# Performance work log

Measured on AMD Instinct MI355X. Metric: run time of the kernel, lower is better.

Reference implementation:

```python
import jax, jax.numpy as jnp
import numpy as np

CAPACITY_FACTOR = 1.0

def setup_inputs() -> dict:
    key = jax.random.key(0)
    ks = jax.random.split(key, 5)
    B, S, D, E, F = 2, 2048, 1024, 8, 4096
    x = jax.random.normal(ks[0], (B, S, D), dtype=jnp.float32)
    Ws = jax.random.normal(ks[1], (D, E), dtype=jnp.float32) * (1.0 / np.sqrt(D))
    bs = jnp.zeros((E,), dtype=jnp.float32)
    W1 = jax.random.normal(ks[2], (E, D, F), dtype=jnp.float32) * (1.0 / np.sqrt(D))
    b1 = jnp.zeros((E, F), dtype=jnp.float32)
    W2 = jax.random.normal(ks[3], (E, F, D), dtype=jnp.float32) * (1.0 / np.sqrt(F))
    b2 = jnp.zeros((E, D), dtype=jnp.float32)
    return {"x": x, "Ws": Ws, "bs": bs, "W1": W1, "b1": b1, "W2": W2, "b2": b2}

def reference(x, Ws, bs, W1, b1, W2, b2):
    B, S, D = x.shape
    E = Ws.shape[1]
    N = B * S
    k = int(CAPACITY_FACTOR * N / E)  # expert-choice capacity
    xf = x.reshape(N, D)
    # switch gating: [N, E] -> [E, N]
    route_prob = jax.nn.softmax(xf @ Ws + bs, axis=-1).T
    # expert-choice top-k tokens per expert: values/indices [E, k]
    route_vals, routes = jax.lax.top_k(route_prob, k)
    # dispatch: gather per-expert token blocks [E, k, D]
    xin = xf[routes]
    # per-expert FFN (grouped GEMM): Linear -> GELU -> Linear
    h = jax.nn.gelu(jnp.einsum('ekd,edf->ekf', xin, W1) + b1[:, None, :])
    out = jnp.einsum('ekf,efd->ekd', h, W2) + b2[:, None, :]
    # scale by routing prob (is_scale_prob=True)
    out = out * route_vals[..., None]
    # combine: scatter-add into token buffer (== sum over the E-indexed zero tensor)
    final = jnp.zeros((N, D), dtype=x.dtype).at[routes.reshape(-1)].add(out.reshape(-1, D))
    return final.reshape(B, S, D)
```

## Files before the change

### kernel.cpp

```cpp
#include <hip/hip_runtime.h>
#include <hip/hip_bf16.h>

#define N_TOK 4096
#define DIM   1024
#define NEXP  8
#define FDIM  4096
#define KCAP  512

typedef __attribute__((ext_vector_type(8))) short bf16x8;
typedef __attribute__((ext_vector_type(4))) float floatx4;

__device__ inline unsigned short f2bf(float f) {
  union { float f; unsigned int i; } v; v.f = f;
  unsigned int r = v.i + 0x7fffu + ((v.i >> 16) & 1u);
  return (unsigned short)(r >> 16);
}

__device__ inline void ld2lds16(const void* g, void* l) {
  __builtin_amdgcn_global_load_lds(
      (const __attribute__((address_space(1))) unsigned int*)g,
      (__attribute__((address_space(3))) unsigned int*)l,
      16, 0, 0);
}

__device__ inline void transpose64(const float* __restrict__ src,
                                   unsigned short* __restrict__ dst,
                                   int R, int C, int e, int by, int bx, int t,
                                   unsigned short (*tile)[66]) {
  size_t off = (size_t)e * R * C;
  int r0 = by * 64, c0 = bx * 64;
  const float* S = src + off + (size_t)r0 * C + c0;
#pragma unroll
  for (int p = 0; p < 4; p++) {
    int r = (t >> 4) + p * 16, c = (t & 15) * 4;
    float4 v = *(const float4*)&S[(size_t)r * C + c];
    tile[r][c + 0] = f2bf(v.x);
    tile[r][c + 1] = f2bf(v.y);
    tile[r][c + 2] = f2bf(v.z);
    tile[r][c + 3] = f2bf(v.w);
  }
  __syncthreads();
  unsigned short* D = dst + off + (size_t)c0 * R + r0;
#pragma unroll
  for (int p = 0; p < 2; p++) {
    int oc = (t >> 3) + p * 32;
    int orr = (t & 7) * 8;
    bf16x8 o;
#pragma unroll
    for (int j = 0; j < 8; j++) o[j] = (short)tile[orr + j][oc];
    *(bf16x8*)&D[(size_t)oc * R + orr] = o;
  }
}

__global__ __launch_bounds__(256)
void prep_kernel(const float* __restrict__ x,
                 const float* __restrict__ Ws,
                 const float* __restrict__ bs,
                 float* __restrict__ probs_t,
                 unsigned short* __restrict__ xb,
                 const float* __restrict__ W1, unsigned short* __restrict__ wt) {
  __shared__ unsigned short tile[64][66];
  int bid = blockIdx.x;
  int t = threadIdx.x;

  if (bid >= 1024) {
    int b = bid - 1024;
    int e = b >> 10, rem = b & 1023;
    int bx = rem & 63, by = rem >> 6;
    transpose64(W1, wt, DIM, FDIM, e, by, bx, t, tile);
    return;
  }

  int token = bid * 4 + (t >> 6);
  int lane  = t & 63;
  const float* xr = x + (size_t)token * DIM;
  unsigned short* xbr = xb + (size_t)token * DIM;
  double acc[NEXP];
#pragma unroll
  for (int e = 0; e < NEXP; e++) acc[e] = 0.0;
#pragma unroll
  for (int c = 0; c < 4; c++) {
    int d0 = (c * 64 + lane) * 4;
    float4 xv = *(const float4*)&xr[d0];
    ushort4 ob;
    ob.x = f2bf(xv.x); ob.y = f2bf(xv.y); ob.z = f2bf(xv.z); ob.w = f2bf(xv.w);
    *(ushort4*)&xbr[d0] = ob;
    float xa[4] = {xv.x, xv.y, xv.z, xv.w};
#pragma unroll
    for (int q = 0; q < 4; q++) {
      const float* wr = &Ws[(size_t)(d0 + q) * NEXP];
      float4 w0 = *(const float4*)&wr[0];
      float4 w1 = *(const float4*)&wr[4];
      double xs = (double)xa[q];
      acc[0] += xs * (double)w0.x; acc[1] += xs * (double)w0.y;
      acc[2] += xs * (double)w0.z; acc[3] += xs * (double)w0.w;
      acc[4] += xs * (double)w1.x; acc[5] += xs * (double)w1.y;
      acc[6] += xs * (double)w1.z; acc[7] += xs * (double)w1.w;
    }
  }
#pragma unroll
  for (int off = 32; off > 0; off >>= 1)
#pragma unroll
    for (int e = 0; e < NEXP; e++) acc[e] += __shfl_down(acc[e], off, 64);
  if (lane == 0) {
    double mx = -1e300;
#pragma unroll
    for (int e = 0; e < NEXP; e++) { acc[e] += (double)bs[e]; if (acc[e] > mx) mx = acc[e]; }
    double s = 0.0, p[NEXP];
#pragma unroll
    for (int e = 0; e < NEXP; e++) { p[e] = exp(acc[e] - mx); s += p[e]; }
#pragma unroll
    for (int e = 0; e < NEXP; e++) probs_t[(size_t)e * N_TOK + token] = (float)(p[e] / s);
  }
}

__global__ __launch_bounds__(256)
void t2_kernel(const float* __restrict__ W2, unsigned short* __restrict__ wt) {
  __shared__ unsigned short tile[64][66];
  int b = blockIdx.x, t = threadIdx.x;
  int e = b >> 10, rem = b & 1023;
  int bx = rem & 15, by = rem >> 4;
  transpose64(W2, wt, FDIM, DIM, e, by, bx, t, tile);
}

__global__ __launch_bounds__(1024)
void topk_kernel(const float* __restrict__ probs_t, int* __restrict__ routes,
                 float* __restrict__ vals, int* __restrict__ counts,
                 int* __restrict__ inv) {
  int e = blockIdx.x;
  const float* P = probs_t + (size_t)e * N_TOK;
  __shared__ int hist[4096];
  __shared__ int hist2[4096];
  __shared__ int scan[1024];
  __shared__ int sB, sR, sCnt;
  __shared__ unsigned int sPrefix, sMask;
  int t = threadIdx.x;

  float vv[4];
  unsigned int vb[4];
  float4 v4 = *(const float4*)&P[t * 4];
  vv[0] = v4.x; vv[1] = v4.y; vv[2] = v4.z; vv[3] = v4.w;
#pragma unroll
  for (int q = 0; q < 4; q++) vb[q] = __float_as_uint(vv[q]);

  if (t == 0) { sR = KCAP; sPrefix = 0u; sMask = 0u; sCnt = 0; }
  __syncthreads();

  for (int level = 0; level < 3; level++) {
    int nb    = (level < 2) ? 4096 : 256;
    int shift = (level == 0) ? 20 : (level == 1) ? 8 : 0;
    for (int i = t; i < nb; i += 1024) hist[i] = 0;
    __syncthreads();
    unsigned int msk = sMask, pfx = sPrefix;
#pragma unroll
    for (int q = 0; q < 4; q++)
      if ((vb[q] & msk) == pfx)
        atomicAdd(&hist[(vb[q] >> shift) & (nb - 1)], 1);
    __syncthreads();
    int* src = hist; int* dst = hist2;
    for (int d = 1; d < nb; d <<= 1) {
      for (int i = t; i < nb; i += 1024)
        dst[i] = src[i] + ((i + d < nb) ? src[i + d] : 0);
      int* tmp = src; src = dst; dst = tmp;
      __syncthreads();
    }
    int R = sR;
    for (int i = t; i < nb; i += 1024) {
      int si = src[i];
      int sn = (i + 1 < nb) ? src[i + 1] : 0;
      if (si >= R && sn < R) sB = i;
    }
    __syncthreads();
    if (t == 0) {
      int B = sB;
      int strict = (B + 1 < nb) ? src[B + 1] : 0;
      sR = sR - strict;
      sPrefix |= ((unsigned int)B) << shift;
      sMask   |= ((unsigned int)(nb - 1)) << shift;
    }
    __syncthreads();
  }

  unsigned int T = sPrefix;
  int R = sR;
  int cnt = 0;
#pragma unroll
  for (int q = 0; q < 4; q++) if (vb[q] == T) cnt++;
  scan[t] = cnt;
  __syncthreads();
  for (int d = 1; d < 1024; d <<= 1) {
    int v = (t >= d) ? scan[t - d] : 0;
    __syncthreads();
    scan[t] += v;
    __syncthreads();
  }
  int grank = scan[t] - cnt;
#pragma unroll
  for (int q = 0; q < 4; q++) {
    bool sel = false;
    if (vb[q] > T) sel = true;
    else if (vb[q] == T) { if (grank < R) sel = true; grank++; }
    if (sel) {
      int pos = atomicAdd(&sCnt, 1);
      int slot = e * KCAP + pos;
      int token = t * 4 + q;
      routes[slot] = token;
      vals[slot]   = vv[q];
      int pc = atomicAdd(&counts[token], 1);
      inv[token * NEXP + pc] = slot;
    }
  }
}

__global__ __launch_bounds__(256, 3)
void gemm1_kernel(const unsigned short* __restrict__ xb,
                  const unsigned short* __restrict__ w1t,
                  const float* __restrict__ b1,
                  const int* __restrict__ routes,
                  unsigned short* __restrict__ h) {
  int lb = blockIdx.x;
  int sb = ((lb & 7) << 7) | (lb >> 3);
  int nt = sb & 31, mt = (sb >> 5) & 3, e = sb >> 7;
  __shared__ unsigned short smem[16384];
  unsigned short* As = smem;
  unsigned short* Bs = smem + 8192;
  int t = threadIdx.x, lane = t & 63, wave = t >> 6;
  int wm = (wave >> 1) * 64, wn = (wave & 1) * 64;
  int fr = lane & 15, fq = lane >> 4;
  int lrow = lane >> 3, lchunk = (lane & 7) ^ (lrow & 7);
  int sw = fr & 7;

  const unsigned short* aP[4];
  const unsigned short* bP[4];
#pragma unroll
  for (int q = 0; q < 4; q++) {
    int m = wave * 4 + q;
    int row = m * 8 + lrow;
    int token = routes[e * KCAP + mt * 128 + row];
    aP[q] = xb + (size_t)token * DIM + lchunk * 8;
    bP[q] = w1t + ((size_t)e * FDIM + nt * 128 + row) * DIM + lchunk * 8;
  }

  floatx4 acc[4][4];
#pragma unroll
  for (int i = 0; i < 4; i++)
#pragma unroll
    for (int j = 0; j < 4; j++) acc[i][j] = (floatx4)0.0f;

  for (int k0 = 0; k0 < DIM; k0 += 64) {
    __syncthreads();
#pragma unroll
    for (int q = 0; q < 4; q++) {
      int m = wave * 4 + q;
      ld2lds16(aP[q] + k0, As + m * 512);
      ld2lds16(bP[q] + k0, Bs + m * 512);
    }
    __syncthreads();
#pragma unroll
    for (int ks = 0; ks < 2; ks++) {
      bf16x8 af[4], bf[4];
      int cs = ((ks << 2) | fq) ^ sw;
#pragma unroll
      for (int i = 0; i < 4; i++)
        af[i] = *(const bf16x8*)&As[(wm + i * 16 + fr) * 64 + cs * 8];
#pragma unroll
      for (int j = 0; j < 4; j++)
        bf[j] = *(const bf16x8*)&Bs[(wn + j * 16 + fr) * 64 + cs * 8];
#pragma unroll
      for (int i = 0; i < 4; i++)
#pragma unroll
        for (int j = 0; j < 4; j++)
          acc[i][j] = __builtin_amdgcn_mfma_f32_16x16x32_bf16(af[i], bf[j], acc[i][j], 0, 0, 0);
    }
  }

  float bias[4];
#pragma unroll
  for (int j = 0; j < 4; j++) bias[j] = b1[e * FDIM + nt * 128 + wn + j * 16 + fr];
  float* LC = (float*)smem;
#pragma unroll
  for (int p = 0; p < 2; p++) {
    __syncthreads();
    if ((wn >> 6) == p) {
#pragma unroll
      for (int i = 0; i < 4; i++)
#pragma unroll
        for (int r = 0; r < 4; r++) {
          int lr = wm + i * 16 + fq * 4 + r;
#pragma unroll
          for (int j = 0; j < 4; j++) {
            float v = acc[i][j][r] + bias[j];
            float u = 0.7978845608028654f * (v + 0.044715f * v * v * v);
            LC[lr * 64 + j * 16 + fr] = v * __builtin_amdgcn_rcpf(1.0f + __expf(-2.0f * u));
          }
        }
    }
    __syncthreads();
    int row = t >> 1, ch = (t & 1) * 32;
    size_t hb = (((size_t)e * 64 + nt * 2 + p) * KCAP + mt * 128 + row) * 64 + ch;
    const float* lrow2 = &LC[row * 64 + ch];
#pragma unroll
    for (int qq = 0; qq < 4; qq++) {
      bf16x8 o;
#pragma unroll
      for (int u8 = 0; u8 < 8; u8++) o[u8] = (short)f2bf(lrow2[qq * 8 + u8]);
      *(bf16x8*)&h[hb + qq * 8] = o;
    }
  }
}

__global__ __launch_bounds__(256, 3)
void gemm2_kernel(const unsigned short* __restrict__ h,
                  const unsigned short* __restrict__ w2t,
                  const float* __restrict__ b2,
                  const float* __restrict__ vals,
                  float* __restrict__ partials) {
  int lb = blockIdx.x;
  int sb = ((lb & 7) << 6) | (lb >> 3);
  int nt = sb & 7, mt = (sb >> 3) & 3, z = sb >> 5;
  int e = z >> 1, s = z & 1;
  __shared__ unsigned short smem[16384];
  unsigned short* As = smem;
  unsigned short* Bs = smem + 8192;
  int t = threadIdx.x, lane = t & 63, wave = t >> 6;
  int wm = (wave >> 1) * 64, wn = (wave & 1) * 64;
  int fr = lane & 15, fq = lane >> 4;
  int lrow = lane >> 3, lchunk = (lane & 7) ^ (lrow & 7);
  int sw = fr & 7;

  const unsigned short* aP[4];
  const unsigned short* bP[4];
#pragma unroll
  for (int q = 0; q < 4; q++) {
    int m = wave * 4 + q;
    int row = m * 8 + lrow;
    aP[q] = h + (((size_t)e * 64 + s * 32) * KCAP + mt * 128 + row) * 64 + lchunk * 8;
    bP[q] = w2t + ((size_t)e * DIM + nt * 128 + row) * FDIM + s * 2048 + lchunk * 8;
  }

  floatx4 acc[4][4];
#pragma unroll
  for (int i = 0; i < 4; i++)
#pragma unroll
    for (int j = 0; j < 4; j++) acc[i][j] = (floatx4)0.0f;

  for (int k0 = 0; k0 < 2048; k0 += 64) {
    __syncthreads();
#pragma unroll
    for (int q = 0; q < 4; q++) {
      int m = wave * 4 + q;
      ld2lds16(aP[q] + (size_t)k0 * 512, As + m * 512);
      ld2lds16(bP[q] + k0, Bs + m * 512);
    }
    __syncthreads();
#pragma unroll
    for (int ks = 0; ks < 2; ks++) {
      bf16x8 af[4], bf[4];
      int cs = ((ks << 2) | fq) ^ sw;
#pragma unroll
      for (int i = 0; i < 4; i++)
        af[i] = *(const bf16x8*)&As[(wm + i * 16 + fr) * 64 + cs * 8];
#pragma unroll
      for (int j = 0; j < 4; j++)
        bf[j] = *(const bf16x8*)&Bs[(wn + j * 16 + fr) * 64 + cs * 8];
#pragma unroll
      for (int i = 0; i < 4; i++)
#pragma unroll
        for (int j = 0; j < 4; j++)
          acc[i][j] = __builtin_amdgcn_mfma_f32_16x16x32_bf16(af[i], bf[j], acc[i][j], 0, 0, 0);
    }
  }

  float* LC = (float*)smem;
  float* outp = partials + (size_t)s * N_TOK * DIM;
  int slotbase = e * KCAP + mt * 128;
  float bias[4];
#pragma unroll
  for (int j = 0; j < 4; j++)
    bias[j] = (s == 0) ? b2[e * DIM + nt * 128 + wn + j * 16 + fr] : 0.0f;
#pragma unroll
  for (int p = 0; p < 2; p++) {
    __syncthreads();
    if ((wn >> 6) == p) {
#pragma unroll
      for (int i = 0; i < 4; i++)
#pragma unroll
        for (int r = 0; r < 4; r++) {
          int lr = wm + i * 16 + fq * 4 + r;
          float vs = vals[slotbase + lr];
#pragma unroll
          for (int j = 0; j < 4; j++)
            LC[lr * 64 + j * 16 + fr] = (acc[i][j][r] + bias[j]) * vs;
        }
    }
    __syncthreads();
    int row = t >> 1, ch = (t & 1) * 32;
    float* dst = outp + (size_t)(slotbase + row) * DIM + nt * 128 + p * 64 + ch;
#pragma unroll
    for (int qq = 0; qq < 8; qq++)
      *(float4*)&dst[qq * 4] = *(const float4*)&LC[row * 64 + ch + qq * 4];
  }
}

__global__ __launch_bounds__(256)
void combine_kernel(const float* __restrict__ partials, const int* __restrict__ counts,
                    const int* __restrict__ inv, float* __restrict__ out) {
  int token = blockIdx.x;
  int t = threadIdx.x;
  int c = counts[token];
  float4 acc = {0.f, 0.f, 0.f, 0.f};
  for (int i = 0; i < c; i++) {
    int slot = inv[token * NEXP + i];
    const float* base = partials + (size_t)slot * DIM + t * 4;
#pragma unroll
    for (int s = 0; s < 2; s++) {
      float4 v = *(const float4*)&base[(size_t)s * N_TOK * DIM];
      acc.x += v.x; acc.y += v.y; acc.z += v.z; acc.w += v.w;
    }
  }
  *(float4*)&out[(size_t)token * DIM + t * 4] = acc;
}

extern "C" void kernel_launch(void* const* d_in, const int* in_sizes, int n_in,
                              void* d_out, int out_size, void* d_ws, size_t ws_size,
                              hipStream_t stream) {
  const float* x  = (const float*)d_in[0];
  const float* Ws = (const float*)d_in[1];
  const float* bs = (const float*)d_in[2];
  const float* W1 = (const float*)d_in[3];
  const float* b1 = (const float*)d_in[4];
  const float* W2 = (const float*)d_in[5];
  const float* b2 = (const float*)d_in[6];
  float* out = (float*)d_out;

  char* ws = (char*)d_ws;
  unsigned short* wt = (unsigned short*)ws; ws += (size_t)NEXP * FDIM * DIM * 2;
  unsigned short* h  = (unsigned short*)ws; ws += (size_t)NEXP * KCAP * FDIM * 2;
  char* pshare = ws; ws += (size_t)2 * N_TOK * DIM * 4;
  unsigned short* xb = (unsigned short*)pshare;
  float* partials    = (float*)pshare;
  float* probs  = (float*)ws; ws += (size_t)NEXP * N_TOK * 4;
  int*   routes = (int*)ws;   ws += NEXP * KCAP * 4;
  float* vals   = (float*)ws; ws += NEXP * KCAP * 4;
  int*   counts = (int*)ws;   ws += N_TOK * 4;
  int*   inv    = (int*)ws;   ws += N_TOK * NEXP * 4;

  hipMemsetAsync(counts, 0, N_TOK * sizeof(int), stream);
  prep_kernel<<<1024 + 8192, 256, 0, stream>>>(x, Ws, bs, probs, xb, W1, wt);
  topk_kernel<<<NEXP, 1024, 0, stream>>>(probs, routes, vals, counts, inv);
  gemm1_kernel<<<1024, 256, 0, stream>>>(xb, wt, b1, routes, h);
  t2_kernel<<<8192, 256, 0, stream>>>(W2, wt);
  gemm2_kernel<<<512, 256, 0, stream>>>(h, wt, b2, vals, partials);
  combine_kernel<<<N_TOK, 256, 0, stream>>>(partials, counts, inv, out);
}
```

Before: 440.7 us.

## Replace 64x64 weight transposes with 256x256 swizzled-LDS transpose kernel

The fp32-to-bf16 weight transpose for W1 and W2 now runs in a dedicated kernel that transposes 256x256 tiles per 512-thread block, staging them in 128KB of LDS with an XOR swizzle in place of padding. The router work is split out of the fused prep kernel into its own launch. The aim is fewer, larger blocks with fully coalesced wide stores and no LDS bank conflicts for this bandwidth-bound conversion. The cost is one extra kernel launch and at most one block per CU because of the large LDS allocation, which may limit latency hiding.

```diff
diff --git a/kernel.cpp b/kernel.cpp
--- a/kernel.cpp
+++ b/kernel.cpp
@@ -23,55 +23,55 @@
       16, 0, 0);
 }
 
-__device__ inline void transpose64(const float* __restrict__ src,
-                                   unsigned short* __restrict__ dst,
-                                   int R, int C, int e, int by, int bx, int t,
-                                   unsigned short (*tile)[66]) {
+__global__ __launch_bounds__(512, 1)
+void tbig_kernel(const float* __restrict__ src, unsigned short* __restrict__ dst,
+                 int R, int C, int ncb) {
+  __shared__ unsigned short tile[65536];
+  int t = threadIdx.x;
+  int bid = blockIdx.x;
+  int e = bid >> 6, rem = bid & 63;
+  int rb = rem / ncb, cb = rem - rb * ncb;
   size_t off = (size_t)e * R * C;
-  int r0 = by * 64, c0 = bx * 64;
+  int r0 = rb * 256, c0 = cb * 256;
   const float* S = src + off + (size_t)r0 * C + c0;
-#pragma unroll
-  for (int p = 0; p < 4; p++) {
-    int r = (t >> 4) + p * 16, c = (t & 15) * 4;
-    float4 v = *(const float4*)&S[(size_t)r * C + c];
-    tile[r][c + 0] = f2bf(v.x);
-    tile[r][c + 1] = f2bf(v.y);
-    tile[r][c + 2] = f2bf(v.z);
-    tile[r][c + 3] = f2bf(v.w);
+  unsigned short* D = dst + off + (size_t)c0 * R + r0;
+
+  int wd = t >> 6;
+  int f0 = (t & 63) * 4;
+  unsigned int* t32 = (unsigned int*)tile;
+#pragma unroll 4
+  for (int p = 0; p < 32; p++) {
+    int d = p * 8 + wd;
+    float4 v = *(const float4*)&S[(size_t)d * C + f0];
+    unsigned int s = ((unsigned int)(d >> 3) & 31u) << 1;
+    unsigned int lo = (unsigned int)f2bf(v.x) | ((unsigned int)f2bf(v.y) << 16);
+    unsigned int hi = (unsigned int)f2bf(v.z) | ((unsigned int)f2bf(v.w) << 16);
+    t32[(d * 256 + (f0 ^ s)) >> 1] = lo;
+    t32[(d * 256 + ((f0 + 2) ^ s)) >> 1] = hi;
   }
   __syncthreads();
-  unsigned short* D = dst + off + (size_t)c0 * R + r0;
-#pragma unroll
-  for (int p = 0; p < 2; p++) {
-    int oc = (t >> 3) + p * 32;
-    int orr = (t & 7) * 8;
+  int d0 = (t & 31) * 8;
+  unsigned int s = ((unsigned int)(t & 31)) << 1;
+  int fl = t >> 5;
+#pragma unroll 4
+  for (int j = 0; j < 16; j++) {
+    int f = j * 16 + fl;
+    int base = d0 * 256 + (f ^ (int)s);
     bf16x8 o;
 #pragma unroll
-    for (int j = 0; j < 8; j++) o[j] = (short)tile[orr + j][oc];
-    *(bf16x8*)&D[(size_t)oc * R + orr] = o;
+    for (int u = 0; u < 8; u++) o[u] = (short)tile[base + u * 256];
+    *(bf16x8*)&D[(size_t)f * R + d0] = o;
   }
 }
 
 __global__ __launch_bounds__(256)
-void prep_kernel(const float* __restrict__ x,
-                 const float* __restrict__ Ws,
-                 const float* __restrict__ bs,
-                 float* __restrict__ probs_t,
-                 unsigned short* __restrict__ xb,
-                 const float* __restrict__ W1, unsigned short* __restrict__ wt) {
-  __shared__ unsigned short tile[64][66];
-  int bid = blockIdx.x;
+void router_kernel(const float* __restrict__ x,
+                   const float* __restrict__ Ws,
+                   const float* __restrict__ bs,
+                   float* __restrict__ probs_t,
+                   unsigned short* __restrict__ xb) {
   int t = threadIdx.x;
-
-  if (bid >= 1024) {
-    int b = bid - 1024;
-    int e = b >> 10, rem = b & 1023;
-    int bx = rem & 63, by = rem >> 6;
-    transpose64(W1, wt, DIM, FDIM, e, by, bx, t, tile);
-    return;
-  }
-
-  int token = bid * 4 + (t >> 6);
+  int token = blockIdx.x * 4 + (t >> 6);
   int lane  = t & 63;
   const float* xr = x + (size_t)token * DIM;
   unsigned short* xbr = xb + (size_t)token * DIM;
@@ -112,15 +112,6 @@
 #pragma unroll
     for (int e = 0; e < NEXP; e++) probs_t[(size_t)e * N_TOK + token] = (float)(p[e] / s);
   }
-}
-
-__global__ __launch_bounds__(256)
-void t2_kernel(const float* __restrict__ W2, unsigned short* __restrict__ wt) {
-  __shared__ unsigned short tile[64][66];
-  int b = blockIdx.x, t = threadIdx.x;
-  int e = b >> 10, rem = b & 1023;
-  int bx = rem & 15, by = rem >> 4;
-  transpose64(W2, wt, FDIM, DIM, e, by, bx, t, tile);
 }
 
 __global__ __launch_bounds__(1024)
@@ -446,10 +437,11 @@
   int*   inv    = (int*)ws;   ws += N_TOK * NEXP * 4;
 
   hipMemsetAsync(counts, 0, N_TOK * sizeof(int), stream);
-  prep_kernel<<<1024 + 8192, 256, 0, stream>>>(x, Ws, bs, probs, xb, W1, wt);
+  tbig_kernel<<<512, 512, 0, stream>>>(W1, wt, DIM, FDIM, 16);
+  router_kernel<<<1024, 256, 0, stream>>>(x, Ws, bs, probs, xb);
   topk_kernel<<<NEXP, 1024, 0, stream>>>(probs, routes, vals, counts, inv);
   gemm1_kernel<<<1024, 256, 0, stream>>>(xb, wt, b1, routes, h);
-  t2_kernel<<<8192, 256, 0, stream>>>(W2, wt);
+  tbig_kernel<<<512, 512, 0, stream>>>(W2, wt, FDIM, DIM, 4);
   gemm2_kernel<<<512, 256, 0, stream>>>(h, wt, b2, vals, partials);
   combine_kernel<<<N_TOK, 256, 0, stream>>>(partials, counts, inv, out);
 }
```

Measured after the change: 460.5 us. +4.5%, slower.
